# Optimization experiments

Hardware: AMD Instinct MI355X
Metric: run time of the kernel (lower is better)

## Reference

```python
import jax, jax.numpy as jnp
import numpy as np

HEADS = 4
LOCAL_CTX = 8  # local_attn_ctx (stride)


def _strided_transpose(x, n_ctx, local_ctx):
    # [B, n_ctx, E] -> reshape [B, n_ctx//local, local, E] -> swap -> [B, n_ctx, E]
    B, _, E = x.shape
    bT = n_ctx // local_ctx
    return x.reshape(B, bT, local_ctx, E).transpose(0, 2, 1, 3).reshape(B, n_ctx, E)


def _strided_untranspose(a, n_ctx, local_ctx):
    B, _, E = a.shape
    bT = n_ctx // local_ctx
    return a.reshape(B, local_ctx, bT, E).transpose(0, 2, 1, 3).reshape(B, n_ctx, E)


def setup_inputs() -> dict:
    key = jax.random.key(0)
    ks = jax.random.split(key, 6)
    B, T, E = 2048, 64, 256
    value = jax.random.normal(ks[0], (B, T, E), dtype=jnp.float32)
    k_in = jax.random.normal(ks[1], (B, T, E), dtype=jnp.float32)
    query = jax.random.normal(ks[2], (B, T, E), dtype=jnp.float32)
    mask = jnp.ones((B, T), dtype=jnp.int32)  # unused by the block
    W_ff = jax.random.normal(ks[3], (256, T * E), dtype=jnp.float32) * (1.0 / np.sqrt(T * E))
    b_ff = jax.random.normal(ks[4], (256,), dtype=jnp.float32) * 0.01
    return {"value": value, "key": k_in, "query": query, "mask": mask, "W_ff": W_ff, "b_ff": b_ff}


def reference(value, key, query, mask, W_ff, b_ff):
    B, n_ctx, E = query.shape
    # strided transpose of q, k, v
    q = _strided_transpose(query, n_ctx, LOCAL_CTX)
    k = _strided_transpose(key, n_ctx, LOCAL_CTX)
    v = _strided_transpose(value, n_ctx, LOCAL_CTX)
    scale = 1.0 / np.sqrt(E // HEADS)  # n_state = embd // heads
    w = jax.nn.softmax(jnp.einsum('bqe,bke->bqk', q, k) * scale, axis=-1)
    a = jnp.einsum('bqk,bke->bqe', w, v)
    attention = _strided_untranspose(a, n_ctx, LOCAL_CTX)
    # residual + dropout (eval-mode identity)
    x = attention + query
    # flatten-linear + ReLU
    out = jax.nn.relu(x.reshape(B, n_ctx * E) @ W_ff.T + b_ff)
    return (out, attention)
```

## Files before the change

### kernel.cpp

```cpp
#include <hip/hip_runtime.h>
#include <stdint.h>

typedef __attribute__((ext_vector_type(8))) short s16x8;
typedef __attribute__((ext_vector_type(4))) float f32x4;

__device__ __forceinline__ unsigned short f2bf(float f) {
  unsigned int u = __float_as_uint(f);
  u += 0x7fffu + ((u >> 16) & 1u);
  return (unsigned short)(u >> 16);
}
__device__ __forceinline__ float bf2f(unsigned short h) {
  return __uint_as_float(((unsigned int)h) << 16);
}
__device__ __forceinline__ f32x4 mfma16(s16x8 a, s16x8 b, f32x4 c) {
  return __builtin_amdgcn_mfma_f32_16x16x32_bf16(a, b, c, 0, 0, 0);
}

__global__ __launch_bounds__(256) void attn_kernel(
    const float* __restrict__ Vg, const float* __restrict__ Kg,
    const float* __restrict__ Qg, float* __restrict__ attn_out,
    unsigned short* __restrict__ xb ) {
  __shared__ __align__(16) char smem[32768];
  char* KhB = smem;
  char* KlB = smem + 16384;
  unsigned short* VtL = (unsigned short*)smem;
  unsigned short* PL = (unsigned short*)(smem + 18432);

  const int b = blockIdx.x;
  const int tid = threadIdx.x;
  const int lane = tid & 63;
  const int w = tid >> 6;
  const int n = lane & 15;
  const int q = lane >> 4;

  const float* Qb = Qg + (size_t)b * 64 * 256;
  const float* Kb = Kg + (size_t)b * 64 * 256;
  const float* Vb = Vg + (size_t)b * 64 * 256;

  f32x4 accS[4];
#pragma unroll
  for (int c = 0; c < 4; ++c) accS[c] = f32x4{0.f, 0.f, 0.f, 0.f};

  float va[16], vbv[16];

  for (int ph = 0; ph < 2; ++ph) {
    const int e0 = ph * 128;
#pragma unroll
    for (int it = 0; it < 8; ++it) {
      int i = it * 256 + tid;
      int row = i >> 5;
      int c4 = i & 31;
      float4 v = *(const float4*)(Kb + row * 256 + e0 + c4 * 4);
      ushort4 hi, lo;
      hi.x = f2bf(v.x); lo.x = f2bf(v.x - bf2f(hi.x));
      hi.y = f2bf(v.y); lo.y = f2bf(v.y - bf2f(hi.y));
      hi.z = f2bf(v.z); lo.z = f2bf(v.z - bf2f(hi.z));
      hi.w = f2bf(v.w); lo.w = f2bf(v.w - bf2f(hi.w));
      int off = row * 256 + ((c4 * 8) ^ ((row & 7) << 4));
      *(ushort4*)(KhB + off) = hi;
      *(ushort4*)(KlB + off) = lo;
    }
    __syncthreads();
    float4 qf0[4], qf1[4];
#pragma unroll
    for (int kk = 0; kk < 4; ++kk) {
      const float* qsrc = Qb + (16 * w + n) * 256 + e0 + kk * 32 + q * 8;
      qf0[kk] = *(const float4*)qsrc;
      qf1[kk] = *(const float4*)(qsrc + 4);
    }
    if (ph == 1) {
#pragma unroll
      for (int i = 0; i < 16; ++i) {
        int j = i * 256 + tid, e = j & 127, tp = j >> 7;
        va[i] = Vb[(2 * tp) * 256 + e];
        vbv[i] = Vb[(2 * tp + 1) * 256 + e];
      }
    }
    __builtin_amdgcn_s_setprio(1);
#pragma unroll
    for (int kk = 0; kk < 4; ++kk) {
      float av[8] = {qf0[kk].x, qf0[kk].y, qf0[kk].z, qf0[kk].w,
                     qf1[kk].x, qf1[kk].y, qf1[kk].z, qf1[kk].w};
      s16x8 qh, ql;
#pragma unroll
      for (int j = 0; j < 8; ++j) {
        unsigned short h = f2bf(av[j]);
        qh[j] = (short)h;
        ql[j] = (short)f2bf(av[j] - bf2f(h));
      }
      const int cb = (kk * 32 + q * 8) * 2;
#pragma unroll
      for (int c = 0; c < 4; ++c) {
        int row = 16 * c + n;
        int off = row * 256 + (cb ^ ((row & 7) << 4));
        s16x8 kh = *(const s16x8*)(KhB + off);
        s16x8 kl = *(const s16x8*)(KlB + off);
        accS[c] = mfma16(qh, kh, accS[c]);
        accS[c] = mfma16(qh, kl, accS[c]);
        accS[c] = mfma16(ql, kh, accS[c]);
      }
    }
    __builtin_amdgcn_s_setprio(0);
    __syncthreads();
  }

  const float scale = 0.125f;
  float p[4][4];
#pragma unroll
  for (int r = 0; r < 4; ++r) {
    float m = -1e30f;
#pragma unroll
    for (int c = 0; c < 4; ++c) m = fmaxf(m, accS[c][r]);
#pragma unroll
    for (int mk = 1; mk < 16; mk <<= 1) m = fmaxf(m, __shfl_xor(m, mk, 64));
    float s = 0.f;
#pragma unroll
    for (int c = 0; c < 4; ++c) {
      float e = __expf((accS[c][r] - m) * scale);
      p[c][r] = e;
      s += e;
    }
#pragma unroll
    for (int mk = 1; mk < 16; mk <<= 1) s += __shfl_xor(s, mk, 64);
    float inv = 1.0f / s;
#pragma unroll
    for (int c = 0; c < 4; ++c) p[c][r] *= inv;
  }

#pragma unroll
  for (int i = 0; i < 16; ++i) {
    int j = i * 256 + tid, e = j & 127, tp = j >> 7;
    unsigned int pk = (unsigned int)f2bf(va[i]) | ((unsigned int)f2bf(vbv[i]) << 16);
    *(unsigned int*)(VtL + e * 72 + 2 * tp) = pk;
  }
#pragma unroll
  for (int r = 0; r < 4; ++r) {
    int row = 16 * w + 4 * q + r;
#pragma unroll
    for (int c = 0; c < 4; ++c) PL[row * 72 + 16 * c + n] = f2bf(p[c][r]);
  }
#pragma unroll
  for (int i = 0; i < 16; ++i) {
    int j = i * 256 + tid, e = j & 127, tp = j >> 7;
    va[i] = Vb[(2 * tp) * 256 + 128 + e];
    vbv[i] = Vb[(2 * tp + 1) * 256 + 128 + e];
  }
  __syncthreads();

  f32x4 accA[16];
#pragma unroll
  for (int c = 0; c < 16; ++c) accA[c] = f32x4{0.f, 0.f, 0.f, 0.f};

  __builtin_amdgcn_s_setprio(1);
#pragma unroll
  for (int ks = 0; ks < 2; ++ks) {
    const int colb = ks * 32 + q * 8;
    s16x8 af = *(const s16x8*)(PL + (16 * w + n) * 72 + colb);
#pragma unroll
    for (int c = 0; c < 8; ++c) {
      s16x8 bf = *(const s16x8*)(VtL + (16 * c + n) * 72 + colb);
      accA[c] = mfma16(af, bf, accA[c]);
    }
  }
  __builtin_amdgcn_s_setprio(0);
  __syncthreads();
#pragma unroll
  for (int i = 0; i < 16; ++i) {
    int j = i * 256 + tid, e = j & 127, tp = j >> 7;
    unsigned int pk = (unsigned int)f2bf(va[i]) | ((unsigned int)f2bf(vbv[i]) << 16);
    *(unsigned int*)(VtL + e * 72 + 2 * tp) = pk;
  }
  __syncthreads();
  __builtin_amdgcn_s_setprio(1);
#pragma unroll
  for (int ks = 0; ks < 2; ++ks) {
    const int colb = ks * 32 + q * 8;
    s16x8 af = *(const s16x8*)(PL + (16 * w + n) * 72 + colb);
#pragma unroll
    for (int c = 8; c < 16; ++c) {
      s16x8 bf = *(const s16x8*)(VtL + (16 * (c - 8) + n) * 72 + colb);
      accA[c] = mfma16(af, bf, accA[c]);
    }
  }
  __builtin_amdgcn_s_setprio(0);

  if (xb) {
#pragma unroll
    for (int h = 0; h < 2; ++h) {
      __syncthreads();
#pragma unroll
      for (int r = 0; r < 4; ++r) {
        int t = 16 * w + 4 * q + r;
        int sw = (t & 7) << 4;
#pragma unroll
        for (int c8 = 0; c8 < 8; ++c8) {
          int c = h * 8 + c8;
          int el = 16 * c8 + n;
          *(float*)(smem + t * 512 + ((el * 4) ^ sw)) = accA[c][r];
        }
      }
      __syncthreads();
#pragma unroll
      for (int i = 0; i < 8; ++i) {
        int f4 = i * 256 + tid;
        int row = f4 >> 5;
        int col4 = f4 & 31;
        int e = h * 128 + col4 * 4;
        float4 av = *(const float4*)(smem + row * 512 + ((col4 * 16) ^ ((row & 7) << 4)));
        float4 qv = *(const float4*)(Qb + row * 256 + e);
        size_t base = ((size_t)b * 64 + row) * 256 + e;
        *(float4*)(attn_out + base) = av;
        ushort4 o;
        o.x = f2bf(av.x + qv.x);
        o.y = f2bf(av.y + qv.y);
        o.z = f2bf(av.z + qv.z);
        o.w = f2bf(av.w + qv.w);
        *(ushort4*)(xb + base) = o;
      }
    }
  } else {
#pragma unroll
    for (int r = 0; r < 4; ++r) {
      int t = 16 * w + 4 * q + r;
      size_t base = ((size_t)b * 64 + t) * 256;
#pragma unroll
      for (int c = 0; c < 16; ++c) attn_out[base + 16 * c + n] = accA[c][r];
    }
  }
}

__global__ __launch_bounds__(256) void w2b_kernel(const float* __restrict__ W,
                                                  unsigned short* __restrict__ Wb) {
  int i = blockIdx.x * 256 + threadIdx.x;
  float4 v = ((const float4*)W)[i];
  ushort4 o;
  o.x = f2bf(v.x); o.y = f2bf(v.y); o.z = f2bf(v.z); o.w = f2bf(v.w);
  ((ushort4*)Wb)[i] = o;
}

template <bool USE_XB>
__global__ __launch_bounds__(256) void ff_kernel(
    const unsigned short* __restrict__ xb, const float* __restrict__ attn,
    const float* __restrict__ query, const unsigned short* __restrict__ Wb,
    float* __restrict__ part, int kchunk) {
  __shared__ __align__(16) unsigned short As[64 * 72];
  __shared__ __align__(16) unsigned short Bs[64 * 72];
  const int tid = threadIdx.x;
  const int lane = tid & 63, w = tid >> 6, n = lane & 15, q = lane >> 4;
  const int m0 = blockIdx.x * 64;
  const int n0 = blockIdx.y * 64;
  const int k0 = blockIdx.z * kchunk;

  f32x4 acc[4];
#pragma unroll
  for (int c = 0; c < 4; ++c) acc[c] = f32x4{0.f, 0.f, 0.f, 0.f};

  const int srow = tid >> 3;
  const int scol = (tid & 7) * 8;

  for (int kk = 0; kk < kchunk; kk += 64) {
#pragma unroll
    for (int rr = 0; rr < 2; ++rr) {
      int row = rr * 32 + srow;
      size_t ga = (size_t)(m0 + row) * 16384 + k0 + kk + scol;
      if (USE_XB) {
        *(uint4*)(As + row * 72 + scol) = *(const uint4*)(xb + ga);
      } else {
        float4 a0 = *(const float4*)(attn + ga);
        float4 a1 = *(const float4*)(attn + ga + 4);
        float4 q0 = *(const float4*)(query + ga);
        float4 q1 = *(const float4*)(query + ga + 4);
        ushort4 h0, h1;
        h0.x = f2bf(a0.x + q0.x); h0.y = f2bf(a0.y + q0.y);
        h0.z = f2bf(a0.z + q0.z); h0.w = f2bf(a0.w + q0.w);
        h1.x = f2bf(a1.x + q1.x); h1.y = f2bf(a1.y + q1.y);
        h1.z = f2bf(a1.z + q1.z); h1.w = f2bf(a1.w + q1.w);
        *(ushort4*)(As + row * 72 + scol) = h0;
        *(ushort4*)(As + row * 72 + scol + 4) = h1;
      }
      size_t gw = (size_t)(n0 + row) * 16384 + k0 + kk + scol;
      *(uint4*)(Bs + row * 72 + scol) = *(const uint4*)(Wb + gw);
    }
    __syncthreads();
#pragma unroll
    for (int ks = 0; ks < 2; ++ks) {
      const int colb = ks * 32 + q * 8;
      s16x8 af = *(const s16x8*)(As + (16 * w + n) * 72 + colb);
#pragma unroll
      for (int c = 0; c < 4; ++c) {
        s16x8 bf = *(const s16x8*)(Bs + (16 * c + n) * 72 + colb);
        acc[c] = mfma16(af, bf, acc[c]);
      }
    }
    __syncthreads();
  }
#pragma unroll
  for (int r = 0; r < 4; ++r) {
    int m = m0 + 16 * w + 4 * q + r;
#pragma unroll
    for (int c = 0; c < 4; ++c) {
      int nn = n0 + 16 * c + n;
      part[((size_t)blockIdx.z * 2048 + m) * 256 + nn] = acc[c][r];
    }
  }
}

__global__ __launch_bounds__(256) void relu_kernel(const float* __restrict__ part,
                                                   const float* __restrict__ bias,
                                                   float* __restrict__ out, int KS) {
  int idx = blockIdx.x * 256 + threadIdx.x;
  float s = bias[idx & 255];
  for (int ks = 0; ks < KS; ++ks) s += part[(size_t)ks * 2048 * 256 + idx];
  out[idx] = fmaxf(s, 0.f);
}

extern "C" void kernel_launch(void* const* d_in, const int* in_sizes, int n_in,
                              void* d_out, int out_size, void* d_ws, size_t ws_size,
                              hipStream_t stream) {
  const float* value = (const float*)d_in[0];
  const float* key   = (const float*)d_in[1];
  const float* query = (const float*)d_in[2];
  const float* W_ff  = (const float*)d_in[4];
  const float* b_ff  = (const float*)d_in[5];

  float* out  = (float*)d_out;
  float* attn = out + (size_t)2048 * 256;

  const int KS = 4;
  const size_t wb_bytes   = (size_t)256 * 16384 * 2;
  const size_t part_bytes = (size_t)KS * 2048 * 256 * 4;
  const size_t xb_bytes   = (size_t)2048 * 64 * 256 * 2;
  unsigned short* Wb = (unsigned short*)d_ws;
  float* part = (float*)((char*)d_ws + wb_bytes);
  bool use_xb = ws_size >= wb_bytes + part_bytes + xb_bytes;
  unsigned short* xb =
      use_xb ? (unsigned short*)((char*)d_ws + wb_bytes + part_bytes) : nullptr;

  w2b_kernel<<<4096, 256, 0, stream>>>(W_ff, Wb);
  attn_kernel<<<2048, 256, 0, stream>>>(value, key, query, attn, xb);
  dim3 gb(32, 4, KS);
  if (use_xb)
    ff_kernel<true><<<gb, 256, 0, stream>>>(xb, nullptr, nullptr, Wb, part, 16384 / KS);
  else
    ff_kernel<false><<<gb, 256, 0, stream>>>(nullptr, attn, query, Wb, part, 16384 / KS);
  relu_kernel<<<2048, 256, 0, stream>>>(part, b_ff, out, KS);
}
```

Before: 262.5 us.

## Load K directly into MFMA fragments and stage full V transpose in LDS

K is no longer staged through LDS as hi/lo bf16 planes. Each lane loads its K fragment straight from global memory and splits it in registers, using truncation for the high part. V is converted during the QK phases into a swizzled transposed LDS layout covering all 256 columns, so the PV product runs in one pass with fewer barriers. Launch bounds now request 4 blocks per CU and LDS use grows to 40 KB. The trade-off is redundant global K reads across waves and higher register and LDS pressure, which could limit occupancy.

Measured after the change: 317.3 us. +20.8%, slower.

```diff
diff --git a/kernel.cpp b/kernel.cpp
--- a/kernel.cpp
+++ b/kernel.cpp
@@ -12,19 +12,19 @@
 __device__ __forceinline__ float bf2f(unsigned short h) {
   return __uint_as_float(((unsigned int)h) << 16);
 }
+__device__ __forceinline__ unsigned short hi_trunc(float f) {
+  return (unsigned short)(__float_as_uint(f) >> 16);
+}
 __device__ __forceinline__ f32x4 mfma16(s16x8 a, s16x8 b, f32x4 c) {
   return __builtin_amdgcn_mfma_f32_16x16x32_bf16(a, b, c, 0, 0, 0);
 }
 
-__global__ __launch_bounds__(256) void attn_kernel(
+__global__ __launch_bounds__(256, 4) void attn_kernel(
     const float* __restrict__ Vg, const float* __restrict__ Kg,
     const float* __restrict__ Qg, float* __restrict__ attn_out,
     unsigned short* __restrict__ xb ) {
-  __shared__ __align__(16) char smem[32768];
-  char* KhB = smem;
-  char* KlB = smem + 16384;
-  unsigned short* VtL = (unsigned short*)smem;
-  unsigned short* PL = (unsigned short*)(smem + 18432);
+  __shared__ __align__(16) char smem[40960];
+  char* PLB = smem + 32768;
 
   const int b = blockIdx.x;
   const int tid = threadIdx.x;
@@ -37,71 +37,68 @@
   const float* Kb = Kg + (size_t)b * 64 * 256;
   const float* Vb = Vg + (size_t)b * 64 * 256;
 
+  const int ve = tid & 127;
+  const int vt0 = tid >> 7;
+
   f32x4 accS[4];
 #pragma unroll
   for (int c = 0; c < 4; ++c) accS[c] = f32x4{0.f, 0.f, 0.f, 0.f};
-
-  float va[16], vbv[16];
 
   for (int ph = 0; ph < 2; ++ph) {
     const int e0 = ph * 128;
-#pragma unroll
-    for (int it = 0; it < 8; ++it) {
-      int i = it * 256 + tid;
-      int row = i >> 5;
-      int c4 = i & 31;
-      float4 v = *(const float4*)(Kb + row * 256 + e0 + c4 * 4);
-      ushort4 hi, lo;
-      hi.x = f2bf(v.x); lo.x = f2bf(v.x - bf2f(hi.x));
-      hi.y = f2bf(v.y); lo.y = f2bf(v.y - bf2f(hi.y));
-      hi.z = f2bf(v.z); lo.z = f2bf(v.z - bf2f(hi.z));
-      hi.w = f2bf(v.w); lo.w = f2bf(v.w - bf2f(hi.w));
-      int off = row * 256 + ((c4 * 8) ^ ((row & 7) << 4));
-      *(ushort4*)(KhB + off) = hi;
-      *(ushort4*)(KlB + off) = lo;
-    }
-    __syncthreads();
-    float4 qf0[4], qf1[4];
+    float vr[4][8];
+#pragma unroll
+    for (int i = 0; i < 4; ++i) {
+      int tg = i * 2 + vt0;
+#pragma unroll
+      for (int j = 0; j < 8; ++j) vr[i][j] = Vb[(tg * 8 + j) * 256 + e0 + ve];
+    }
 #pragma unroll
     for (int kk = 0; kk < 4; ++kk) {
-      const float* qsrc = Qb + (16 * w + n) * 256 + e0 + kk * 32 + q * 8;
-      qf0[kk] = *(const float4*)qsrc;
-      qf1[kk] = *(const float4*)(qsrc + 4);
-    }
-    if (ph == 1) {
-#pragma unroll
-      for (int i = 0; i < 16; ++i) {
-        int j = i * 256 + tid, e = j & 127, tp = j >> 7;
-        va[i] = Vb[(2 * tp) * 256 + e];
-        vbv[i] = Vb[(2 * tp + 1) * 256 + e];
-      }
-    }
-    __builtin_amdgcn_s_setprio(1);
-#pragma unroll
-    for (int kk = 0; kk < 4; ++kk) {
-      float av[8] = {qf0[kk].x, qf0[kk].y, qf0[kk].z, qf0[kk].w,
-                     qf1[kk].x, qf1[kk].y, qf1[kk].z, qf1[kk].w};
+      const int cb = kk * 32 + q * 8;
+      const float* qsrc = Qb + (16 * w + n) * 256 + e0 + cb;
+      float4 q0 = *(const float4*)qsrc;
+      float4 q1 = *(const float4*)(qsrc + 4);
+      float4 k0[4], k1[4];
+#pragma unroll
+      for (int c = 0; c < 4; ++c) {
+        const float* ksrc = Kb + (16 * c + n) * 256 + e0 + cb;
+        k0[c] = *(const float4*)ksrc;
+        k1[c] = *(const float4*)(ksrc + 4);
+      }
+      float qa[8] = {q0.x, q0.y, q0.z, q0.w, q1.x, q1.y, q1.z, q1.w};
       s16x8 qh, ql;
 #pragma unroll
       for (int j = 0; j < 8; ++j) {
-        unsigned short h = f2bf(av[j]);
+        unsigned short h = hi_trunc(qa[j]);
         qh[j] = (short)h;
-        ql[j] = (short)f2bf(av[j] - bf2f(h));
-      }
-      const int cb = (kk * 32 + q * 8) * 2;
+        ql[j] = (short)f2bf(qa[j] - bf2f(h));
+      }
 #pragma unroll
       for (int c = 0; c < 4; ++c) {
-        int row = 16 * c + n;
-        int off = row * 256 + (cb ^ ((row & 7) << 4));
-        s16x8 kh = *(const s16x8*)(KhB + off);
-        s16x8 kl = *(const s16x8*)(KlB + off);
+        float ka[8] = {k0[c].x, k0[c].y, k0[c].z, k0[c].w,
+                       k1[c].x, k1[c].y, k1[c].z, k1[c].w};
+        s16x8 kh, kl;
+#pragma unroll
+        for (int j = 0; j < 8; ++j) {
+          unsigned short h = hi_trunc(ka[j]);
+          kh[j] = (short)h;
+          kl[j] = (short)f2bf(ka[j] - bf2f(h));
+        }
         accS[c] = mfma16(qh, kh, accS[c]);
         accS[c] = mfma16(qh, kl, accS[c]);
         accS[c] = mfma16(ql, kh, accS[c]);
       }
     }
-    __builtin_amdgcn_s_setprio(0);
-    __syncthreads();
+#pragma unroll
+    for (int i = 0; i < 4; ++i) {
+      int tg = i * 2 + vt0;
+      int e = e0 + ve;
+      s16x8 pk;
+#pragma unroll
+      for (int j = 0; j < 8; ++j) pk[j] = (short)f2bf(vr[i][j]);
+      *(s16x8*)(smem + e * 128 + ((tg * 16) ^ ((e & 7) << 4))) = pk;
+    }
   }
 
   const float scale = 0.125f;
@@ -128,57 +125,29 @@
   }
 
 #pragma unroll
-  for (int i = 0; i < 16; ++i) {
-    int j = i * 256 + tid, e = j & 127, tp = j >> 7;
-    unsigned int pk = (unsigned int)f2bf(va[i]) | ((unsigned int)f2bf(vbv[i]) << 16);
-    *(unsigned int*)(VtL + e * 72 + 2 * tp) = pk;
-  }
-#pragma unroll
   for (int r = 0; r < 4; ++r) {
     int row = 16 * w + 4 * q + r;
-#pragma unroll
-    for (int c = 0; c < 4; ++c) PL[row * 72 + 16 * c + n] = f2bf(p[c][r]);
-  }
-#pragma unroll
-  for (int i = 0; i < 16; ++i) {
-    int j = i * 256 + tid, e = j & 127, tp = j >> 7;
-    va[i] = Vb[(2 * tp) * 256 + 128 + e];
-    vbv[i] = Vb[(2 * tp + 1) * 256 + 128 + e];
+    int sw = (row & 7) << 4;
+#pragma unroll
+    for (int c = 0; c < 4; ++c)
+      *(unsigned short*)(PLB + row * 128 + ((2 * (16 * c + n)) ^ sw)) =
+          f2bf(p[c][r]);
   }
   __syncthreads();
 
   f32x4 accA[16];
 #pragma unroll
   for (int c = 0; c < 16; ++c) accA[c] = f32x4{0.f, 0.f, 0.f, 0.f};
-
   __builtin_amdgcn_s_setprio(1);
 #pragma unroll
   for (int ks = 0; ks < 2; ++ks) {
-    const int colb = ks * 32 + q * 8;
-    s16x8 af = *(const s16x8*)(PL + (16 * w + n) * 72 + colb);
-#pragma unroll
-    for (int c = 0; c < 8; ++c) {
-      s16x8 bf = *(const s16x8*)(VtL + (16 * c + n) * 72 + colb);
-      accA[c] = mfma16(af, bf, accA[c]);
-    }
-  }
-  __builtin_amdgcn_s_setprio(0);
-  __syncthreads();
-#pragma unroll
-  for (int i = 0; i < 16; ++i) {
-    int j = i * 256 + tid, e = j & 127, tp = j >> 7;
-    unsigned int pk = (unsigned int)f2bf(va[i]) | ((unsigned int)f2bf(vbv[i]) << 16);
-    *(unsigned int*)(VtL + e * 72 + 2 * tp) = pk;
-  }
-  __syncthreads();
-  __builtin_amdgcn_s_setprio(1);
-#pragma unroll
-  for (int ks = 0; ks < 2; ++ks) {
-    const int colb = ks * 32 + q * 8;
-    s16x8 af = *(const s16x8*)(PL + (16 * w + n) * 72 + colb);
-#pragma unroll
-    for (int c = 8; c < 16; ++c) {
-      s16x8 bf = *(const s16x8*)(VtL + (16 * (c - 8) + n) * 72 + colb);
+    const int cb = (ks * 32 + q * 8) * 2;
+    const int sw = (n & 7) << 4;
+    s16x8 af = *(const s16x8*)(PLB + (16 * w + n) * 128 + (cb ^ sw));
+#pragma unroll
+    for (int c = 0; c < 16; ++c) {
+      int row = 16 * c + n;
+      s16x8 bf = *(const s16x8*)(smem + row * 128 + (cb ^ sw));
       accA[c] = mfma16(af, bf, accA[c]);
     }
   }
@@ -194,9 +163,8 @@
         int sw = (t & 7) << 4;
 #pragma unroll
         for (int c8 = 0; c8 < 8; ++c8) {
-          int c = h * 8 + c8;
           int el = 16 * c8 + n;
-          *(float*)(smem + t * 512 + ((el * 4) ^ sw)) = accA[c][r];
+          *(float*)(smem + t * 512 + ((el * 4) ^ sw)) = accA[h * 8 + c8][r];
         }
       }
       __syncthreads();
```
